# Optimization experiments

Measured on AMD Instinct MI355X. Metric: run time of the kernel, lower is better.

## Reference

```python
import jax, jax.numpy as jnp
import numpy as np

WINDOW = 3  # windows_size


def setup_inputs() -> dict:
    key = jax.random.key(0)
    k1, k2 = jax.random.split(key)
    S, B, H = 200, 1024, 128
    stdv = np.sqrt(2.0 / H)
    inputs = jax.random.normal(k1, (S, B, H), dtype=jnp.float32)
    mask = jnp.ones((S, B), dtype=jnp.float32)
    conv_kernel = jax.random.uniform(k2, (WINDOW, H), dtype=jnp.float32,
                                     minval=-stdv, maxval=stdv)
    return {"inputs": inputs, "mask": mask, "conv_kernel": conv_kernel}


def reference(inputs, mask, conv_kernel):
    # dropout rate is 0.0 -> identity
    S, B, H = inputs.shape
    W = conv_kernel.shape[0]
    x = inputs * mask[:, :, None]                       # [S, B, H]
    pad = jnp.concatenate(
        [x, jnp.zeros((W - 1, B, H), dtype=x.dtype)], axis=0)  # [S+W-1, B, H]
    # Sliding windows along the step axis; W is a small structural constant.
    windows = jnp.stack([pad[i:S + i] for i in range(W)])  # [W, S, B, H]
    # Gated attention score per window offset: sigmoid then dot with kernel row.
    alpha = jnp.einsum('wsbh,wh->wsb', jax.nn.sigmoid(windows), conv_kernel)
    alpha = jax.nn.softmax(alpha, axis=0)               # softmax over window axis
    # Weighted sum over the window axis.
    out = jnp.einsum('wsbh,wsb->sbh', windows, alpha)   # [S, B, H]
    return out
```

## Files before the change

### kernel.cpp

```cpp
#include <hip/hip_runtime.h>


#define S_DIM 200
#define B_DIM 1024
#define H_DIM 128
#define R_STRIP 8
#define BGRPS (B_DIM / 4)
#define STRIPS (S_DIM / R_STRIP)

__device__ __forceinline__ float fast_rcp(float v) {
    return __builtin_amdgcn_rcpf(v);
}

__global__ __launch_bounds__(256) void LocalCAN_kernel(
    const float* __restrict__ x,
    const float* __restrict__ mask,
    const float* __restrict__ ker,
    float* __restrict__ out)
{
    const int wave = (blockIdx.x * blockDim.x + threadIdx.x) >> 6;
    const int lane = threadIdx.x & 63;
    const int bgrp  = wave % BGRPS;
    const int strip = wave / BGRPS;
    if (strip >= STRIPS) return;

    const int bsub = lane >> 4;
    const int hg   = lane & 15;
    const int b    = bgrp * 4 + bsub;
    const int h0   = hg * 4;
    const int s0   = strip * R_STRIP;

    float kr[3][8];
    #pragma unroll
    for (int w = 0; w < 3; ++w) {
        const float4 ka = *reinterpret_cast<const float4*>(&ker[w * H_DIM + h0]);
        const float4 kb = *reinterpret_cast<const float4*>(&ker[w * H_DIM + 64 + h0]);
        kr[w][0] = ka.x; kr[w][1] = ka.y; kr[w][2] = ka.z; kr[w][3] = ka.w;
        kr[w][4] = kb.x; kr[w][5] = kb.y; kr[w][6] = kb.z; kr[w][7] = kb.w;
    }

    float xr[3][8];
    float dr[3][3];

    #pragma unroll
    for (int i = 0; i < R_STRIP + 2; ++i) {
        const int r    = s0 + i;
        const int slot = i % 3;

        float v[8];
        if (r < S_DIM) {
            const float m = mask[r * B_DIM + b];
            const size_t base = ((size_t)r * B_DIM + b) * H_DIM;
            const float4 va = *reinterpret_cast<const float4*>(&x[base + h0]);
            const float4 vb = *reinterpret_cast<const float4*>(&x[base + 64 + h0]);
            v[0] = va.x * m; v[1] = va.y * m; v[2] = va.z * m; v[3] = va.w * m;
            v[4] = vb.x * m; v[5] = vb.y * m; v[6] = vb.z * m; v[7] = vb.w * m;
        } else {
            #pragma unroll
            for (int j = 0; j < 8; ++j) v[j] = 0.f;
        }

        float p0 = 0.f, p1 = 0.f, p2 = 0.f;
        #pragma unroll
        for (int j = 0; j < 8; ++j) {
            const float sg = fast_rcp(1.f + __expf(-v[j]));
            p0 += sg * kr[0][j];
            p1 += sg * kr[1][j];
            p2 += sg * kr[2][j];
            xr[slot][j] = v[j];
        }
        #pragma unroll
        for (int off = 1; off < 16; off <<= 1) {
            p0 += __shfl_xor(p0, off);
            p1 += __shfl_xor(p1, off);
            p2 += __shfl_xor(p2, off);
        }
        dr[slot][0] = p0; dr[slot][1] = p1; dr[slot][2] = p2;

        if (i >= 2) {
            const int so  = r - 2;
            const int sA  = (i - 2) % 3;
            const int sB  = (i - 1) % 3;
            const int sC  = slot;
            const float d0 = dr[sA][0], d1 = dr[sB][1], d2 = dr[sC][2];
            const float mx = fmaxf(d0, fmaxf(d1, d2));
            const float e0 = __expf(d0 - mx);
            const float e1 = __expf(d1 - mx);
            const float e2 = __expf(d2 - mx);
            const float inv = fast_rcp(e0 + e1 + e2);
            const float a0 = e0 * inv, a1 = e1 * inv, a2 = e2 * inv;

            float o[8];
            #pragma unroll
            for (int j = 0; j < 8; ++j)
                o[j] = xr[sA][j] * a0 + xr[sB][j] * a1 + xr[sC][j] * a2;

            const size_t obase = ((size_t)so * B_DIM + b) * H_DIM;
            *reinterpret_cast<float4*>(&out[obase + h0]) =
                make_float4(o[0], o[1], o[2], o[3]);
            *reinterpret_cast<float4*>(&out[obase + 64 + h0]) =
                make_float4(o[4], o[5], o[6], o[7]);
        }
    }
}

extern "C" void kernel_launch(void* const* d_in, const int* in_sizes, int n_in,
                              void* d_out, int out_size, void* d_ws, size_t ws_size,
                              hipStream_t stream) {
    const float* x    = (const float*)d_in[0];
    const float* mask = (const float*)d_in[1];
    const float* ker  = (const float*)d_in[2];
    float* out = (float*)d_out;

    const int total_waves = BGRPS * STRIPS;
    const int threads = 256;
    const int blocks = (total_waves * 64 + threads - 1) / threads;
    LocalCAN_kernel<<<blocks, threads, 0, stream>>>(x, mask, ker, out);
}
```

Measured before the change: 190.2 us.

## Shrink row strips and widen lane mapping, hoisting all loads before compute

Measured after the change: 188.2 us. Within noise of the previous version (-1.1%).

```diff
diff --git a/kernel.cpp b/kernel.cpp
--- a/kernel.cpp
+++ b/kernel.cpp
@@ -4,8 +4,9 @@
 #define S_DIM 200
 #define B_DIM 1024
 #define H_DIM 128
-#define R_STRIP 8
-#define BGRPS (B_DIM / 4)
+#define R_STRIP 4
+#define ROWS (R_STRIP + 2)
+#define BGRPS (B_DIM / 2)
 #define STRIPS (S_DIM / R_STRIP)
 
 __device__ __forceinline__ float fast_rcp(float v) {
@@ -18,89 +19,77 @@
     const float* __restrict__ ker,
     float* __restrict__ out)
 {
-    const int wave = (blockIdx.x * blockDim.x + threadIdx.x) >> 6;
-    const int lane = threadIdx.x & 63;
+    const int wave  = (blockIdx.x * blockDim.x + threadIdx.x) >> 6;
+    const int lane  = threadIdx.x & 63;
     const int bgrp  = wave % BGRPS;
     const int strip = wave / BGRPS;
-    if (strip >= STRIPS) return;
 
-    const int bsub = lane >> 4;
-    const int hg   = lane & 15;
-    const int b    = bgrp * 4 + bsub;
+    const int bsub = lane >> 5;
+    const int hg   = lane & 31;
+    const int b    = bgrp * 2 + bsub;
     const int h0   = hg * 4;
     const int s0   = strip * R_STRIP;
 
-    float kr[3][8];
+    float kr[3][4];
     #pragma unroll
     for (int w = 0; w < 3; ++w) {
-        const float4 ka = *reinterpret_cast<const float4*>(&ker[w * H_DIM + h0]);
-        const float4 kb = *reinterpret_cast<const float4*>(&ker[w * H_DIM + 64 + h0]);
-        kr[w][0] = ka.x; kr[w][1] = ka.y; kr[w][2] = ka.z; kr[w][3] = ka.w;
-        kr[w][4] = kb.x; kr[w][5] = kb.y; kr[w][6] = kb.z; kr[w][7] = kb.w;
+        const float4 k4 = *reinterpret_cast<const float4*>(&ker[w * H_DIM + h0]);
+        kr[w][0] = k4.x; kr[w][1] = k4.y; kr[w][2] = k4.z; kr[w][3] = k4.w;
     }
 
-    float xr[3][8];
-    float dr[3][3];
-
+    float v[ROWS][4];
     #pragma unroll
-    for (int i = 0; i < R_STRIP + 2; ++i) {
-        const int r    = s0 + i;
-        const int slot = i % 3;
-
-        float v[8];
+    for (int i = 0; i < ROWS; ++i) {
+        const int r = s0 + i;
         if (r < S_DIM) {
             const float m = mask[r * B_DIM + b];
-            const size_t base = ((size_t)r * B_DIM + b) * H_DIM;
-            const float4 va = *reinterpret_cast<const float4*>(&x[base + h0]);
-            const float4 vb = *reinterpret_cast<const float4*>(&x[base + 64 + h0]);
-            v[0] = va.x * m; v[1] = va.y * m; v[2] = va.z * m; v[3] = va.w * m;
-            v[4] = vb.x * m; v[5] = vb.y * m; v[6] = vb.z * m; v[7] = vb.w * m;
+            const float4 t = *reinterpret_cast<const float4*>(
+                &x[((size_t)r * B_DIM + b) * H_DIM + h0]);
+            v[i][0] = t.x * m; v[i][1] = t.y * m;
+            v[i][2] = t.z * m; v[i][3] = t.w * m;
         } else {
-            #pragma unroll
-            for (int j = 0; j < 8; ++j) v[j] = 0.f;
+            v[i][0] = v[i][1] = v[i][2] = v[i][3] = 0.f;
         }
+    }
 
+    float d[ROWS][3];
+    #pragma unroll
+    for (int i = 0; i < ROWS; ++i) {
         float p0 = 0.f, p1 = 0.f, p2 = 0.f;
         #pragma unroll
-        for (int j = 0; j < 8; ++j) {
-            const float sg = fast_rcp(1.f + __expf(-v[j]));
+        for (int j = 0; j < 4; ++j) {
+            const float sg = fast_rcp(1.f + __expf(-v[i][j]));
             p0 += sg * kr[0][j];
             p1 += sg * kr[1][j];
             p2 += sg * kr[2][j];
-            xr[slot][j] = v[j];
         }
         #pragma unroll
-        for (int off = 1; off < 16; off <<= 1) {
+        for (int off = 1; off < 32; off <<= 1) {
             p0 += __shfl_xor(p0, off);
             p1 += __shfl_xor(p1, off);
             p2 += __shfl_xor(p2, off);
         }
-        dr[slot][0] = p0; dr[slot][1] = p1; dr[slot][2] = p2;
+        d[i][0] = p0; d[i][1] = p1; d[i][2] = p2;
+    }
 
-        if (i >= 2) {
-            const int so  = r - 2;
-            const int sA  = (i - 2) % 3;
-            const int sB  = (i - 1) % 3;
-            const int sC  = slot;
-            const float d0 = dr[sA][0], d1 = dr[sB][1], d2 = dr[sC][2];
-            const float mx = fmaxf(d0, fmaxf(d1, d2));
-            const float e0 = __expf(d0 - mx);
-            const float e1 = __expf(d1 - mx);
-            const float e2 = __expf(d2 - mx);
-            const float inv = fast_rcp(e0 + e1 + e2);
-            const float a0 = e0 * inv, a1 = e1 * inv, a2 = e2 * inv;
+    #pragma unroll
+    for (int o = 0; o < R_STRIP; ++o) {
+        const float d0 = d[o][0], d1 = d[o + 1][1], d2 = d[o + 2][2];
+        const float mx = fmaxf(d0, fmaxf(d1, d2));
+        const float e0 = __expf(d0 - mx);
+        const float e1 = __expf(d1 - mx);
+        const float e2 = __expf(d2 - mx);
+        const float inv = fast_rcp(e0 + e1 + e2);
+        const float a0 = e0 * inv, a1 = e1 * inv, a2 = e2 * inv;
 
-            float o[8];
-            #pragma unroll
-            for (int j = 0; j < 8; ++j)
-                o[j] = xr[sA][j] * a0 + xr[sB][j] * a1 + xr[sC][j] * a2;
+        float4 ov;
+        ov.x = v[o][0] * a0 + v[o + 1][0] * a1 + v[o + 2][0] * a2;
+        ov.y = v[o][1] * a0 + v[o + 1][1] * a1 + v[o + 2][1] * a2;
+        ov.z = v[o][2] * a0 + v[o + 1][2] * a1 + v[o + 2][2] * a2;
+        ov.w = v[o][3] * a0 + v[o + 1][3] * a1 + v[o + 2][3] * a2;
 
-            const size_t obase = ((size_t)so * B_DIM + b) * H_DIM;
-            *reinterpret_cast<float4*>(&out[obase + h0]) =
-                make_float4(o[0], o[1], o[2], o[3]);
-            *reinterpret_cast<float4*>(&out[obase + 64 + h0]) =
-                make_float4(o[4], o[5], o[6], o[7]);
-        }
+        *reinterpret_cast<float4*>(
+            &out[((size_t)(s0 + o) * B_DIM + b) * H_DIM + h0]) = ov;
     }
 }
 
```
